# Performance work log

Measured on AMD Instinct MI355X. Metric: run time of the kernel, lower is better.

## Reference

```python
import jax, jax.numpy as jnp
import numpy as np

B, S, HIDDEN = 2, 2048, 1024
NUM_HEADS, HEAD_DIM = 16, 64
STRIDE = 128
NEG = -10000.0


def _strided_mask(seq_len):
    # Sparse Transformer strided pattern: causal, local window of STRIDE,
    # plus every STRIDE-th previous position.
    i = jnp.arange(seq_len)[:, None]
    j = jnp.arange(seq_len)[None, :]
    diff = i - j
    allowed = (diff >= 0) & ((diff < STRIDE) | (diff % STRIDE == 0))
    return jnp.where(allowed, 0.0, NEG).astype(jnp.float32)  # [S, S]


def setup_inputs() -> dict:
    key = jax.random.key(0)
    k0, k1, k2, k3, k4 = jax.random.split(key, 5)
    hidden_states = jax.random.normal(k0, (B, S, HIDDEN), dtype=jnp.float32)
    attention_mask = jnp.zeros((B, 1, 1, S), dtype=jnp.float32)
    W_q = jax.random.normal(k1, (HIDDEN, HIDDEN), dtype=jnp.float32) * 0.02
    b_q = jnp.zeros((HIDDEN,), dtype=jnp.float32)
    W_v = jax.random.normal(k2, (HIDDEN, HIDDEN), dtype=jnp.float32) * 0.02
    b_v = jnp.zeros((HIDDEN,), dtype=jnp.float32)
    return {"hidden_states": hidden_states, "attention_mask": attention_mask,
            "W_q": W_q, "b_q": b_q, "W_v": W_v, "b_v": b_v}


def _heads(x):
    b, s, _ = x.shape
    return x.reshape(b, s, NUM_HEADS, HEAD_DIM).transpose(0, 2, 1, 3)  # [B,H,S,d]


def reference(hidden_states, attention_mask, W_q, b_q, W_v, b_v):
    q = _heads(hidden_states @ W_q + b_q)  # [B,H,S,d]
    v = _heads(hidden_states @ W_v + b_v)  # [B,H,S,d]
    hash_mask = _strided_mask(q.shape[-2])  # [S,S], broadcast over B,H
    # NB: source computes matmul(query, query^T) -- Q used for both sides.
    scores = jnp.einsum('bhid,bhjd->bhij', q, q) + hash_mask
    scores = scores / jnp.sqrt(jnp.asarray(HEAD_DIM, scores.dtype))
    scores = scores + attention_mask
    probs = jax.nn.softmax(scores, axis=-1)  # dropout p=0 (eval)
    ctx = jnp.einsum('bhij,bhjd->bhid', probs, v)  # [B,H,S,d]
    b = ctx.shape[0]
    return ctx.transpose(0, 2, 1, 3).reshape(b, -1, NUM_HEADS * HEAD_DIM)
```

## Files before the change

### kernel.cpp

```cpp
#include <hip/hip_runtime.h>

typedef __attribute__((ext_vector_type(8))) short short8;
typedef __attribute__((ext_vector_type(4))) float float4v;

__device__ inline float bf2f(ushort u) {
    unsigned v = ((unsigned)u) << 16;
    return __builtin_bit_cast(float, v);
}
__device__ inline ushort f2bf(float f) {
    unsigned u = __builtin_bit_cast(unsigned, f);
    u += 0x7FFFu + ((u >> 16) & 1u);
    return (ushort)(u >> 16);
}

__device__ inline void gload_lds16(const ushort* g, ushort* l) {
    __builtin_amdgcn_global_load_lds(
        (const __attribute__((address_space(1))) unsigned int*)g,
        (__attribute__((address_space(3))) unsigned int*)l,
        16, 0, 0);
}

__global__ __launch_bounds__(256) void convert_hs(
    const float* __restrict__ hs, ushort* __restrict__ hsb) {
    const size_t base = ((size_t)blockIdx.x * 256 + threadIdx.x) * 16;
    union { ushort u[16]; uint4 v[2]; } o;
#pragma unroll
    for (int q = 0; q < 4; ++q) {
        float4v f = *(const float4v*)(hs + base + q * 4);
#pragma unroll
        for (int j = 0; j < 4; ++j) o.u[q * 4 + j] = f2bf(f[j]);
    }
    *(uint4*)(hsb + base)     = o.v[0];
    *(uint4*)(hsb + base + 8) = o.v[1];
}

__global__ __launch_bounds__(256) void transpose_w(
    const float* __restrict__ Wq, const float* __restrict__ Wv,
    ushort* __restrict__ Wtq, ushort* __restrict__ Wtv) {
    __shared__ ushort tile[64][68];
    const float* W = blockIdx.z ? Wv : Wq;
    ushort* Wt     = blockIdx.z ? Wtv : Wtq;
    const int k0 = blockIdx.y * 64, n0 = blockIdx.x * 64;
    const int tid = threadIdx.x;
    const int rr = tid >> 4;
    const int cc = (tid & 15) * 4;
    union U4 { ushort u[4]; uint2 v; };
#pragma unroll
    for (int i = 0; i < 4; ++i) {
        int row = rr + i * 16;
        float4v f = *(const float4v*)(W + (size_t)(k0 + row) * 1024 + n0 + cc);
        U4 x;
#pragma unroll
        for (int j = 0; j < 4; ++j) x.u[j] = f2bf(f[j]);
        *(uint2*)&tile[row][cc] = x.v;
    }
    __syncthreads();
#pragma unroll
    for (int i = 0; i < 4; ++i) {
        int row = rr + i * 16;
        U4 o;
#pragma unroll
        for (int j = 0; j < 4; ++j) o.u[j] = tile[cc + j][row];
        *(uint2*)(Wt + (size_t)(n0 + row) * 1024 + k0 + cc) = o.v;
    }
}

__global__ __launch_bounds__(256) void qv_gemm(
    const ushort* __restrict__ hsb,
    const ushort* __restrict__ Wtq, const ushort* __restrict__ Wtv,
    const float* __restrict__ bq, const float* __restrict__ bv,
    ushort* __restrict__ q_ws, ushort* __restrict__ v_ws) {
    __shared__ ushort Al[128 * 64];
    __shared__ ushort Bl[128 * 64];
    const ushort* Wt  = blockIdx.z ? Wtv : Wtq;
    const float* bias = blockIdx.z ? bv : bq;
    ushort* out       = blockIdx.z ? v_ws : q_ws;
    const int m0 = blockIdx.y * 128, n0 = blockIdx.x * 128;
    const int tid = threadIdx.x;
    const int wid = tid >> 6, lane = tid & 63;
    const int quad = lane >> 4, l16 = lane & 15;
    const int wm = (wid >> 1) * 64, wn = (wid & 1) * 64;
    const int rbase = 32 * wid;
    const int srow = lane >> 3, scol = (lane & 7) * 8;

    float4v acc[4][4] = {};

    for (int kt = 0; kt < 1024; kt += 64) {
        __syncthreads();
#pragma unroll
        for (int c8 = 0; c8 < 4; ++c8) {
            int row = rbase + c8 * 8;
            gload_lds16(hsb + (size_t)(m0 + row + srow) * 1024 + kt + scol,
                        &Al[row * 64]);
            gload_lds16(Wt + (size_t)(n0 + row + srow) * 1024 + kt + scol,
                        &Bl[row * 64]);
        }
        __syncthreads();
#pragma unroll
        for (int ks = 0; ks < 2; ++ks) {
            short8 af[4], bfr[4];
#pragma unroll
            for (int mt = 0; mt < 4; ++mt)
                af[mt] = *(const short8*)&Al[(wm + mt * 16 + l16) * 64 + (ks * 4 + quad) * 8];
#pragma unroll
            for (int nt = 0; nt < 4; ++nt)
                bfr[nt] = *(const short8*)&Bl[(wn + nt * 16 + l16) * 64 + (ks * 4 + quad) * 8];
#pragma unroll
            for (int mt = 0; mt < 4; ++mt)
#pragma unroll
                for (int nt = 0; nt < 4; ++nt)
                    acc[mt][nt] = __builtin_amdgcn_mfma_f32_16x16x32_bf16(
                        af[mt], bfr[nt], acc[mt][nt], 0, 0, 0);
        }
    }
#pragma unroll
    for (int mt = 0; mt < 4; ++mt) {
#pragma unroll
        for (int nt = 0; nt < 4; ++nt) {
            int coln = n0 + wn + nt * 16 + l16;
            float bsv = bias[coln];
            int hh = coln >> 6, dd = coln & 63;
#pragma unroll
            for (int reg = 0; reg < 4; ++reg) {
                int r = m0 + wm + mt * 16 + quad * 4 + reg;
                int bb = r >> 11, s = r & 2047;
                out[(((size_t)bb * 16 + hh) * 2048 + s) * 64 + dd] =
                    f2bf(acc[mt][nt][reg] + bsv);
            }
        }
    }
}

__global__ __launch_bounds__(512, 4) void attn(
    const ushort* __restrict__ q_ws, const ushort* __restrict__ v_ws,
    const float* __restrict__ amask, float* __restrict__ out) {
    const int t = blockIdx.x, h = blockIdx.y, b = blockIdx.z;

    __shared__ ushort KwPl[16384];
    __shared__ ushort VtS[16384];
    __shared__ float  Sstr[128][17];
    __shared__ float  amw[256];

    const int tid = threadIdx.x;
    const int wid = tid >> 6, lane = tid & 63;
    const int quad = lane >> 4, l16 = lane & 15;
    const int r0 = wid * 16;
    const size_t qbase = ((size_t)b * 16 + h) * 2048 * 64;
    const int base_row = (t - 1) * 128;
    const int nk = (t >= 2) ? (t - 1) : 0;

    if (tid < 256) {
        int j = base_row + tid; if (j < 0) j = 0;
        amw[tid] = amask[(size_t)b * 2048 + j];
    }
#pragma unroll
    for (int i = 0; i < 4; ++i) {
        int u = tid + i * 512;
        int row = u >> 3, c = u & 7;
        int jg = base_row + row; if (jg < 0) jg = 0;
        *(uint4*)&KwPl[row * 64 + ((c ^ (row & 7)) * 8)] =
            *(const uint4*)(q_ws + qbase + (size_t)jg * 64 + c * 8);
    }
    {
        int j = tid & 255, dh0 = (tid >> 8) * 32;
        int jg = base_row + j; if (jg < 0) jg = 0;
        const ushort* src = v_ws + qbase + (size_t)jg * 64 + dh0;
        int cj = j >> 3, j7 = j & 7;
#pragma unroll
        for (int d = 0; d < 32; d += 8) {
            union { uint4 v; ushort u[8]; } tmp;
            tmp.v = *(const uint4*)(src + d);
#pragma unroll
            for (int jj = 0; jj < 8; ++jj) {
                int dd = dh0 + d + jj;
                VtS[dd * 256 + ((cj ^ (dd & 7)) * 8) + j7] = tmp.u[jj];
            }
        }
    }
    __syncthreads();

    float4v sacc[16] = {};
#pragma unroll
    for (int ks = 0; ks < 2; ++ks) {
        int c = ks * 4 + quad;
        int sw = (c ^ (l16 & 7)) * 8;
        short8 af = *(const short8*)&KwPl[(128 + r0 + l16) * 64 + sw];
#pragma unroll
        for (int nt = 0; nt < 16; ++nt) {
            short8 bfr = *(const short8*)&KwPl[(nt * 16 + l16) * 64 + sw];
            sacc[nt] = __builtin_amdgcn_mfma_f32_16x16x32_bf16(af, bfr, sacc[nt], 0, 0, 0);
        }
    }

    const int sr = tid >> 2;
    const int dq = (tid & 3) * 16;
    if (nk > 0) {
        float qv[16];
#pragma unroll
        for (int cc = 0; cc < 2; ++cc) {
            int c = (dq >> 3) + cc;
            union { uint4 v; ushort u[8]; } tm;
            tm.v = *(const uint4*)&KwPl[(128 + sr) * 64 + ((c ^ (sr & 7)) * 8)];
#pragma unroll
            for (int jj = 0; jj < 8; ++jj) qv[cc * 8 + jj] = bf2f(tm.u[jj]);
        }
        for (int k = 0; k < nk; ++k) {
            const ushort* kr = q_ws + qbase + (size_t)(sr + (k << 7)) * 64 + dq;
            float p = 0.f;
#pragma unroll
            for (int d = 0; d < 16; d += 8) {
                union { uint4 v; ushort u[8]; } tm;
                tm.v = *(const uint4*)(kr + d);
#pragma unroll
                for (int jj = 0; jj < 8; ++jj) p += qv[d + jj] * bf2f(tm.u[jj]);
            }
            p += __shfl_xor(p, 1);
            p += __shfl_xor(p, 2);
            if ((tid & 3) == 0)
                Sstr[sr][k] = p * 0.125f + amask[(size_t)b * 2048 + sr + (k << 7)];
        }
    }
    __syncthreads();

    unsigned pb[4][4];
#pragma unroll
    for (int reg = 0; reg < 4; ++reg) {
        int rr = r0 + quad * 4 + reg;
        float sv[16];
#pragma unroll
        for (int nt = 0; nt < 16; ++nt) {
            int c = nt * 16 + l16;
            bool allowed = (c >= rr) && (c <= rr + 128) && (t > 0 || c >= 128);
            sv[nt] = allowed ? sacc[nt][reg] * 0.125f + amw[c] : -INFINITY;
        }
        float sstr_v = (l16 < nk) ? Sstr[rr][l16] : -INFINITY;
        float m = sstr_v;
#pragma unroll
        for (int nt = 0; nt < 16; ++nt) m = fmaxf(m, sv[nt]);
#pragma unroll
        for (int off = 1; off < 16; off <<= 1) m = fmaxf(m, __shfl_xor(m, off));

        float es = (l16 < nk) ? __expf(sstr_v - m) : 0.f;
        float sum = es;
#pragma unroll
        for (int nt = 0; nt < 16; ++nt) {
            float e = (sv[nt] == -INFINITY) ? 0.f : __expf(sv[nt] - m);
            sv[nt] = e; sum += e;
        }
#pragma unroll
        for (int off = 1; off < 16; off <<= 1) sum += __shfl_xor(sum, off);
        float rden = 1.f / sum;
#pragma unroll
        for (int nt = 0; nt < 8; ++nt) {
            int c = nt * 2 + (l16 >> 3);
            KwPl[rr * 128 + ((c ^ (rr & 15)) * 8) + (l16 & 7)] = f2bf(sv[nt] * rden);
        }
#pragma unroll
        for (int i2 = 0; i2 < 4; ++i2) {
            unsigned lo = f2bf(sv[8 + 2 * i2] * rden);
            unsigned hi = f2bf(sv[9 + 2 * i2] * rden);
            pb[reg][i2] = lo | (hi << 16);
        }
        if (l16 < nk) Sstr[rr][l16] = es * rden;
    }
    __syncthreads();

    float4v cacc[4] = {};
#pragma unroll
    for (int ks = 0; ks < 4; ++ks) {
        int cp = ks * 4 + quad;
        short8 af = *(const short8*)&KwPl[(r0 + l16) * 128 + ((cp ^ l16) * 8)];
#pragma unroll
        for (int nt = 0; nt < 4; ++nt) {
            int sw = (cp ^ (l16 & 7)) * 8;
            short8 bfr = *(const short8*)&VtS[(nt * 16 + l16) * 256 + sw];
            cacc[nt] = __builtin_amdgcn_mfma_f32_16x16x32_bf16(af, bfr, cacc[nt], 0, 0, 0);
        }
    }
    __syncthreads();

#pragma unroll
    for (int reg = 0; reg < 4; ++reg) {
        int rr = r0 + quad * 4 + reg;
#pragma unroll
        for (int i2 = 0; i2 < 4; ++i2) {
            int nt0 = 8 + 2 * i2;
#pragma unroll
            for (int e2 = 0; e2 < 2; ++e2) {
                int nt = nt0 + e2;
                int c = (nt - 8) * 2 + (l16 >> 3);
                ushort val = (ushort)((pb[reg][i2] >> (16 * e2)) & 0xFFFF);
                KwPl[rr * 128 + ((c ^ (rr & 15)) * 8) + (l16 & 7)] = val;
            }
        }
    }
    __syncthreads();

#pragma unroll
    for (int ks = 0; ks < 4; ++ks) {
        int cp = ks * 4 + quad;
        short8 af = *(const short8*)&KwPl[(r0 + l16) * 128 + ((cp ^ l16) * 8)];
#pragma unroll
        for (int nt = 0; nt < 4; ++nt) {
            int cv = 16 + cp;
            int sw = (cv ^ (l16 & 7)) * 8;
            short8 bfr = *(const short8*)&VtS[(nt * 16 + l16) * 256 + sw];
            cacc[nt] = __builtin_amdgcn_mfma_f32_16x16x32_bf16(af, bfr, cacc[nt], 0, 0, 0);
        }
    }
    __syncthreads();

    float* ctxp = (float*)&VtS[0];
    {
        float acc16[16] = {};
        for (int k = 0; k < nk; ++k) {
            float p = Sstr[sr][k];
            const ushort* vr = v_ws + qbase + (size_t)(sr + (k << 7)) * 64 + dq;
#pragma unroll
            for (int d = 0; d < 16; d += 8) {
                union { uint4 v; ushort u[8]; } tm;
                tm.v = *(const uint4*)(vr + d);
#pragma unroll
                for (int jj = 0; jj < 8; ++jj) acc16[d + jj] += p * bf2f(tm.u[jj]);
            }
        }
#pragma unroll
        for (int d4 = 0; d4 < 4; ++d4) {
            int c = (dq >> 2) + d4;
            *(float4v*)&ctxp[sr * 64 + ((c ^ (sr & 15)) * 4)] =
                *(const float4v*)&acc16[d4 * 4];
        }
    }
    __syncthreads();

    const size_t obase = ((size_t)b * 2048 + (size_t)t * 128) * 1024 + (size_t)h * 64;
#pragma unroll
    for (int nt = 0; nt < 4; ++nt)
#pragma unroll
        for (int reg = 0; reg < 4; ++reg) {
            int rr = r0 + quad * 4 + reg;
            int d = nt * 16 + l16;
            float cstr = ctxp[rr * 64 + (((d >> 2) ^ (rr & 15)) * 4) + (d & 3)];
            out[obase + (size_t)rr * 1024 + d] = cacc[nt][reg] + cstr;
        }
}

extern "C" void kernel_launch(void* const* d_in, const int* in_sizes, int n_in,
                              void* d_out, int out_size, void* d_ws, size_t ws_size,
                              hipStream_t stream) {
    int ihs = -1, iam = -1, iw1 = -1, iw2 = -1, ib1 = -1, ib2 = -1;
    for (int i = 0; i < n_in; ++i) {
        int s = in_sizes[i];
        if      (s == 4194304) { if (ihs < 0) ihs = i; }
        else if (s == 4096)    { if (iam < 0) iam = i; }
        else if (s == 1048576) { if (iw1 < 0) iw1 = i; else if (iw2 < 0) iw2 = i; }
        else if (s == 1024)    { if (ib1 < 0) ib1 = i; else if (ib2 < 0) ib2 = i; }
    }
    if (ihs < 0) ihs = 0; if (iam < 0) iam = 1;
    if (iw1 < 0) iw1 = 2; if (ib1 < 0) ib1 = 3;
    if (iw2 < 0) iw2 = 4; if (ib2 < 0) ib2 = 5;

    const float* hs    = (const float*)d_in[ihs];
    const float* amask = (const float*)d_in[iam];
    const float* Wq    = (const float*)d_in[iw1];
    const float* bq    = (const float*)d_in[ib1];
    const float* Wv    = (const float*)d_in[iw2];
    const float* bv    = (const float*)d_in[ib2];
    float* out = (float*)d_out;

    char* ws = (char*)d_ws;
    ushort* Wtq  = (ushort*)(ws);
    ushort* Wtv  = (ushort*)(ws + (1u << 21));
    ushort* hsb  = (ushort*)(ws + (2u << 21));
    ushort* q_ws = (ushort*)(ws + (2u << 21) + (1u << 23));
    ushort* v_ws = (ushort*)(ws + (2u << 21) + (2u << 23));

    convert_hs<<<1024, 256, 0, stream>>>(hs, hsb);
    transpose_w<<<dim3(16, 16, 2), 256, 0, stream>>>(Wq, Wv, Wtq, Wtv);
    qv_gemm<<<dim3(8, 32, 2), 256, 0, stream>>>(hsb, Wtq, Wtv, bq, bv, q_ws, v_ws);
    attn<<<dim3(16, 16, 2), 512, 0, stream>>>(q_ws, v_ws, amask, out);
}
```

Before: 149.7 us.

## Skip masked attention tiles, stage GEMM epilogue through LDS, vectorize V transpose

```diff
diff --git a/kernel.cpp b/kernel.cpp
--- a/kernel.cpp
+++ b/kernel.cpp
@@ -70,8 +70,9 @@
     const ushort* __restrict__ Wtq, const ushort* __restrict__ Wtv,
     const float* __restrict__ bq, const float* __restrict__ bv,
     ushort* __restrict__ q_ws, ushort* __restrict__ v_ws) {
-    __shared__ ushort Al[128 * 64];
-    __shared__ ushort Bl[128 * 64];
+    __shared__ ushort S[2 * 128 * 64];
+    ushort* Al = S;
+    ushort* Bl = S + 128 * 64;
     const ushort* Wt  = blockIdx.z ? Wtv : Wtq;
     const float* bias = blockIdx.z ? bv : bq;
     ushort* out       = blockIdx.z ? v_ws : q_ws;
@@ -113,20 +114,33 @@
                         af[mt], bfr[nt], acc[mt][nt], 0, 0, 0);
         }
     }
+    __syncthreads();
 #pragma unroll
     for (int mt = 0; mt < 4; ++mt) {
 #pragma unroll
         for (int nt = 0; nt < 4; ++nt) {
-            int coln = n0 + wn + nt * 16 + l16;
-            float bsv = bias[coln];
-            int hh = coln >> 6, dd = coln & 63;
+            int col = wn + nt * 16 + l16;
+            float bsv = bias[n0 + col];
 #pragma unroll
             for (int reg = 0; reg < 4; ++reg) {
-                int r = m0 + wm + mt * 16 + quad * 4 + reg;
-                int bb = r >> 11, s = r & 2047;
-                out[(((size_t)bb * 16 + hh) * 2048 + s) * 64 + dd] =
+                int row = wm + mt * 16 + quad * 4 + reg;
+                S[row * 128 + (((col >> 3) ^ (row & 15)) << 3) + (col & 7)] =
                     f2bf(acc[mt][nt][reg] + bsv);
             }
+        }
+    }
+    __syncthreads();
+    {
+        int row = tid >> 1, half = tid & 1;
+        int r = m0 + row;
+        int bb = r >> 11, s = r & 2047;
+        int hh = (n0 >> 6) + half;
+        ushort* dst = out + (((size_t)bb * 16 + hh) * 2048 + s) * 64;
+#pragma unroll
+        for (int c8 = 0; c8 < 8; ++c8) {
+            int chunk = half * 8 + c8;
+            *(uint4*)(dst + c8 * 8) =
+                *(const uint4*)&S[row * 128 + ((chunk ^ (row & 15)) << 3)];
         }
     }
 }
@@ -148,6 +162,9 @@
     const size_t qbase = ((size_t)b * 16 + h) * 2048 * 64;
     const int base_row = (t - 1) * 128;
     const int nk = (t >= 2) ? (t - 1) : 0;
+    const int lo = wid & ~1;
+    const int cklo = wid >> 1;
+    const int ckhi = (wid * 16 + 143) >> 5;
 
     if (tid < 256) {
         int j = base_row + tid; if (j < 0) j = 0;
@@ -162,19 +179,21 @@
             *(const uint4*)(q_ws + qbase + (size_t)jg * 64 + c * 8);
     }
     {
-        int j = tid & 255, dh0 = (tid >> 8) * 32;
-        int jg = base_row + j; if (jg < 0) jg = 0;
-        const ushort* src = v_ws + qbase + (size_t)jg * 64 + dh0;
-        int cj = j >> 3, j7 = j & 7;
-#pragma unroll
-        for (int d = 0; d < 32; d += 8) {
-            union { uint4 v; ushort u[8]; } tmp;
-            tmp.v = *(const uint4*)(src + d);
-#pragma unroll
-            for (int jj = 0; jj < 8; ++jj) {
-                int dd = dh0 + d + jj;
-                VtS[dd * 256 + ((cj ^ (dd & 7)) * 8) + j7] = tmp.u[jj];
-            }
+        int j0 = (tid & 63) * 4, d0 = (tid >> 6) * 8;
+        ushort vreg[4][8];
+#pragma unroll
+        for (int jj = 0; jj < 4; ++jj) {
+            int jg = base_row + j0 + jj; if (jg < 0) jg = 0;
+            *(uint4*)vreg[jj] = *(const uint4*)(v_ws + qbase + (size_t)jg * 64 + d0);
+        }
+        int cj = j0 >> 3, j7 = j0 & 7;
+#pragma unroll
+        for (int dd8 = 0; dd8 < 8; ++dd8) {
+            int dd = d0 + dd8;
+            union { ushort u4[4]; uint2 v; } pk;
+            pk.u4[0] = vreg[0][dd8]; pk.u4[1] = vreg[1][dd8];
+            pk.u4[2] = vreg[2][dd8]; pk.u4[3] = vreg[3][dd8];
+            *(uint2*)&VtS[dd * 256 + ((cj ^ (dd & 7)) * 8) + j7] = pk.v;
         }
     }
     __syncthreads();
@@ -187,8 +206,10 @@
         short8 af = *(const short8*)&KwPl[(128 + r0 + l16) * 64 + sw];
 #pragma unroll
         for (int nt = 0; nt < 16; ++nt) {
-            short8 bfr = *(const short8*)&KwPl[(nt * 16 + l16) * 64 + sw];
-            sacc[nt] = __builtin_amdgcn_mfma_f32_16x16x32_bf16(af, bfr, sacc[nt], 0, 0, 0);
+            if (nt >= wid && nt <= wid + 8) {
+                short8 bfr = *(const short8*)&KwPl[(nt * 16 + l16) * 64 + sw];
+                sacc[nt] = __builtin_amdgcn_mfma_f32_16x16x32_bf16(af, bfr, sacc[nt], 0, 0, 0);
+            }
         }
     }
 
@@ -229,9 +250,11 @@
         float sv[16];
 #pragma unroll
         for (int nt = 0; nt < 16; ++nt) {
-            int c = nt * 16 + l16;
-            bool allowed = (c >= rr) && (c <= rr + 128) && (t > 0 || c >= 128);
-            sv[nt] = allowed ? sacc[nt][reg] * 0.125f + amw[c] : -INFINITY;
+            if (nt >= wid && nt <= wid + 8) {
+                int c = nt * 16 + l16;
+                bool allowed = (c >= rr) && (c <= rr + 128) && (t > 0 || c >= 128);
+                sv[nt] = allowed ? sacc[nt][reg] * 0.125f + amw[c] : -INFINITY;
+            } else sv[nt] = -INFINITY;
         }
         float sstr_v = (l16 < nk) ? Sstr[rr][l16] : -INFINITY;
         float m = sstr_v;
@@ -252,14 +275,16 @@
         float rden = 1.f / sum;
 #pragma unroll
         for (int nt = 0; nt < 8; ++nt) {
-            int c = nt * 2 + (l16 >> 3);
-            KwPl[rr * 128 + ((c ^ (rr & 15)) * 8) + (l16 & 7)] = f2bf(sv[nt] * rden);
+            if (nt >= lo && nt <= lo + 9) {
+                int c = nt * 2 + (l16 >> 3);
+                KwPl[rr * 128 + ((c ^ (rr & 15)) * 8) + (l16 & 7)] = f2bf(sv[nt] * rden);
+            }
         }
 #pragma unroll
         for (int i2 = 0; i2 < 4; ++i2) {
-            unsigned lo = f2bf(sv[8 + 2 * i2] * rden);
-            unsigned hi = f2bf(sv[9 + 2 * i2] * rden);
-            pb[reg][i2] = lo | (hi << 16);
+            unsigned plo = f2bf(sv[8 + 2 * i2] * rden);
+            unsigned phi = f2bf(sv[9 + 2 * i2] * rden);
+            pb[reg][i2] = plo | (phi << 16);
         }
         if (l16 < nk) Sstr[rr][l16] = es * rden;
     }
@@ -268,13 +293,15 @@
     float4v cacc[4] = {};
 #pragma unroll
     for (int ks = 0; ks < 4; ++ks) {
-        int cp = ks * 4 + quad;
-        short8 af = *(const short8*)&KwPl[(r0 + l16) * 128 + ((cp ^ l16) * 8)];
-#pragma unroll
-        for (int nt = 0; nt < 4; ++nt) {
-            int sw = (cp ^ (l16 & 7)) * 8;
-            short8 bfr = *(const short8*)&VtS[(nt * 16 + l16) * 256 + sw];
-            cacc[nt] = __builtin_amdgcn_mfma_f32_16x16x32_bf16(af, bfr, cacc[nt], 0, 0, 0);
+        if (ks >= cklo && ks <= ckhi) {
+            int cp = ks * 4 + quad;
+            short8 af = *(const short8*)&KwPl[(r0 + l16) * 128 + ((cp ^ l16) * 8)];
+#pragma unroll
+            for (int nt = 0; nt < 4; ++nt) {
+                int sw = (cp ^ (l16 & 7)) * 8;
+                short8 bfr = *(const short8*)&VtS[(nt * 16 + l16) * 256 + sw];
+                cacc[nt] = __builtin_amdgcn_mfma_f32_16x16x32_bf16(af, bfr, cacc[nt], 0, 0, 0);
+            }
         }
     }
     __syncthreads();
@@ -284,13 +311,14 @@
         int rr = r0 + quad * 4 + reg;
 #pragma unroll
         for (int i2 = 0; i2 < 4; ++i2) {
-            int nt0 = 8 + 2 * i2;
 #pragma unroll
             for (int e2 = 0; e2 < 2; ++e2) {
-                int nt = nt0 + e2;
-                int c = (nt - 8) * 2 + (l16 >> 3);
-                ushort val = (ushort)((pb[reg][i2] >> (16 * e2)) & 0xFFFF);
-                KwPl[rr * 128 + ((c ^ (rr & 15)) * 8) + (l16 & 7)] = val;
+                int nt = 8 + 2 * i2 + e2;
+                if (nt >= lo && nt <= lo + 9) {
+                    int c = (nt - 8) * 2 + (l16 >> 3);
+                    ushort val = (ushort)((pb[reg][i2] >> (16 * e2)) & 0xFFFF);
+                    KwPl[rr * 128 + ((c ^ (rr & 15)) * 8) + (l16 & 7)] = val;
+                }
             }
         }
     }
@@ -298,14 +326,16 @@
 
 #pragma unroll
     for (int ks = 0; ks < 4; ++ks) {
-        int cp = ks * 4 + quad;
-        short8 af = *(const short8*)&KwPl[(r0 + l16) * 128 + ((cp ^ l16) * 8)];
-#pragma unroll
-        for (int nt = 0; nt < 4; ++nt) {
-            int cv = 16 + cp;
-            int sw = (cv ^ (l16 & 7)) * 8;
-            short8 bfr = *(const short8*)&VtS[(nt * 16 + l16) * 256 + sw];
-            cacc[nt] = __builtin_amdgcn_mfma_f32_16x16x32_bf16(af, bfr, cacc[nt], 0, 0, 0);
+        if (4 + ks >= cklo && 4 + ks <= ckhi) {
+            int cp = ks * 4 + quad;
+            short8 af = *(const short8*)&KwPl[(r0 + l16) * 128 + ((cp ^ l16) * 8)];
+#pragma unroll
+            for (int nt = 0; nt < 4; ++nt) {
+                int cv = 16 + cp;
+                int sw = (cv ^ (l16 & 7)) * 8;
+                short8 bfr = *(const short8*)&VtS[(nt * 16 + l16) * 256 + sw];
+                cacc[nt] = __builtin_amdgcn_mfma_f32_16x16x32_bf16(af, bfr, cacc[nt], 0, 0, 0);
+            }
         }
     }
     __syncthreads();
```

Result: slower. 153.6 us (+2.6%).
